# Kernel optimization log

Measured on AMD Instinct MI355X. Metric: run time of the kernel, lower is better.

## Reference

```python
import jax, jax.numpy as jnp
import numpy as np

N = 512      # state dim n
K = 8        # num_regimes
H = 256      # hidden dim for g0/g1/gate MLPs
B = 8192     # batch
INIT_SCALE = 0.1


def _mlp(x, w1, b1, w2, b2, w3, b3):
    # 2 hidden SiLU layers + linear head (matches ScalarMLP/GateNet with num_layers=2)
    h = jax.nn.silu(x @ w1 + b1)
    h = jax.nn.silu(h @ w2 + b2)
    return h @ w3 + b3


def setup_inputs() -> dict:
    key = jax.random.key(0)
    ks = jax.random.split(key, 12)

    def lin(k, fi, fo):
        kw, kb = jax.random.split(k)
        s = 1.0 / np.sqrt(fi)  # torch nn.Linear default init range
        w = jax.random.uniform(kw, (fi, fo), minval=-s, maxval=s, dtype=jnp.float32)
        b = jax.random.uniform(kb, (fo,), minval=-s, maxval=s, dtype=jnp.float32)
        return w, b

    g0_w1, g0_b1 = lin(ks[0], N, H)
    g0_w2, g0_b2 = lin(ks[1], H, H)
    g0_w3, g0_b3 = lin(ks[2], H, 1)
    g1_w1, g1_b1 = lin(ks[3], N, H)
    g1_w2, g1_b2 = lin(ks[4], H, H)
    g1_w3, g1_b3 = lin(ks[5], H, 1)
    gt_w1, gt_b1 = lin(ks[6], N, H)
    gt_w2, gt_b2 = lin(ks[7], H, H)
    gt_w3, gt_b3 = lin(ks[8], H, K)
    W = jax.random.uniform(ks[9], (K, N, N), minval=-INIT_SCALE, maxval=INIT_SCALE, dtype=jnp.float32)
    z = jax.random.normal(ks[10], (B, 2 * N), dtype=jnp.float32)
    return dict(z=z,
                g0_w1=g0_w1, g0_b1=g0_b1, g0_w2=g0_w2, g0_b2=g0_b2, g0_w3=g0_w3, g0_b3=g0_b3,
                g1_w1=g1_w1, g1_b1=g1_b1, g1_w2=g1_w2, g1_b2=g1_b2, g1_w3=g1_w3, g1_b3=g1_b3,
                gt_w1=gt_w1, gt_b1=gt_b1, gt_w2=gt_w2, gt_b2=gt_b2, gt_w3=gt_w3, gt_b3=gt_b3,
                W=W)


def reference(z,
              g0_w1, g0_b1, g0_w2, g0_b2, g0_w3, g0_b3,
              g1_w1, g1_b1, g1_w2, g1_b2, g1_w3, g1_b3,
              gt_w1, gt_b1, gt_w2, gt_b2, gt_w3, gt_b3,
              W):
    n = W.shape[-1]
    x0, x1 = z[:, :n], z[:, n:]

    def U(x0_, x1_):
        e0 = jnp.sum(_mlp(x0_, g0_w1, g0_b1, g0_w2, g0_b2, g0_w3, g0_b3))  # scalar
        e1 = jnp.sum(_mlp(x1_, g1_w1, g1_b1, g1_w2, g1_b2, g1_w3, g1_b3))
        alpha = jax.nn.softmax(_mlp(x0_, gt_w1, gt_b1, gt_w2, gt_b2, gt_w3, gt_b3), axis=-1)  # [B,K]
        # per-sample per-regime bilinear x1^T W_k x0 -> avoids materializing [B,n,n] W_eff
        q = jnp.einsum('bi,kij,bj->bk', x1_, W, x0_)
        return e0 + e1 + jnp.sum(alpha * q)

    grad_x0, grad_x1 = jax.grad(U, argnums=(0, 1))(x0, x1)
    return jnp.concatenate([-grad_x0, -grad_x1], axis=-1)  # [B, 2n]
```

## Files before the change

kernel.cpp:

```cpp
#include <hip/hip_runtime.h>
#include <cstdint>
#include <cstddef>

constexpr int BTOT = 8192, N = 512, H = 256, K = 8;

typedef __attribute__((ext_vector_type(8))) short short8v;
typedef __attribute__((ext_vector_type(4))) float f32x4;

__device__ __forceinline__ float bf2f(unsigned short u) {
    return __uint_as_float(((uint32_t)u) << 16);
}
__device__ __forceinline__ unsigned short f2bf(float f) {
    uint32_t u = __float_as_uint(f);
    uint32_t r = (u + 0x7FFFu + ((u >> 16) & 1u)) >> 16;
    return (unsigned short)r;
}

typedef __attribute__((address_space(3))) unsigned int lds_uint;
typedef __attribute__((address_space(1))) const unsigned int glob_uint;
__device__ __forceinline__ void async16(const unsigned short* g, unsigned short* l) {
    __builtin_amdgcn_global_load_lds((glob_uint*)g, (lds_uint*)l, 16, 0, 0);
}

struct GArg {
    const unsigned short* A;
    const unsigned short* Bt;
    const float* bias;
    const float* w3v;
    const unsigned short* dmul;
    unsigned short* ob;
    unsigned short* ob2;
    float* of;
    float* qout;
    const unsigned short* xq;
    int lda, ldbt, Ka, lddm, ldob, ldof;
};

enum { EPI_BF = 0, EPI_FWD = 1, EPI_BWD2 = 2, EPI_NEG = 3, EPI_NEGW = 4 };

template<int EPI>
__global__ __launch_bounds__(256) void gemm_g(GArg ga0, GArg ga1, GArg ga2)
{
    const int z = blockIdx.z;
    const GArg g = (z == 0) ? ga0 : (z == 1) ? ga1 : ga2;

    __shared__ __attribute__((aligned(16))) unsigned short As[3 * 128 * 32];
    __shared__ __attribute__((aligned(16))) unsigned short Bs[3 * 128 * 32];
    const int tid = threadIdx.x;
    const int lane = tid & 63, wave = tid >> 6;
    const int m0 = blockIdx.y * 128, n0 = blockIdx.x * 128;
    const int wr = (wave >> 1) * 64, wc = (wave & 1) * 64;
    const int rr = lane & 15;
    const int kb = ((lane >> 4) ^ (lane & 3)) << 3;

    const int r0 = tid >> 2;
    const int ko0 = (((tid & 3) ^ (r0 & 3)) << 3);
    const unsigned short* gA0 = g.A + (size_t)(m0 + r0) * g.lda + ko0;
    const unsigned short* gA1 = g.A + (size_t)(m0 + r0 + 64) * g.lda + ko0;
    const unsigned short* gB0 = g.Bt + (size_t)(n0 + r0) * g.ldbt + ko0;
    const unsigned short* gB1 = g.Bt + (size_t)(n0 + r0 + 64) * g.ldbt + ko0;

    auto stage = [&](int t, int buf) {
        const int k0 = t << 5;
        async16(gA0 + k0, As + buf * 4096 + tid * 8);
        async16(gA1 + k0, As + buf * 4096 + (tid + 256) * 8);
        async16(gB0 + k0, Bs + buf * 4096 + tid * 8);
        async16(gB1 + k0, Bs + buf * 4096 + (tid + 256) * 8);
    };

    f32x4 acc[4][4];
    #pragma unroll
    for (int i = 0; i < 4; ++i)
        #pragma unroll
        for (int j = 0; j < 4; ++j) acc[i][j] = (f32x4){0.f, 0.f, 0.f, 0.f};

    const int nt = g.Ka >> 5;

    stage(0, 0);
    if (nt > 1) stage(1, 1);

    int buf = 0;
    for (int t = 0; t < nt; ++t) {
        if (t + 1 < nt) { asm volatile("s_waitcnt vmcnt(4)" ::: "memory"); }
        else            { asm volatile("s_waitcnt vmcnt(0)" ::: "memory"); }
        __builtin_amdgcn_s_barrier();
        if (t + 2 < nt) {
            int b2 = buf + 2; if (b2 >= 3) b2 -= 3;
            stage(t + 2, b2);
        }
        short8v af[4], bfr[4];
        #pragma unroll
        for (int i = 0; i < 4; ++i)
            af[i] = *(const short8v*)(As + buf * 4096 + (wr + i * 16 + rr) * 32 + kb);
        #pragma unroll
        for (int j = 0; j < 4; ++j)
            bfr[j] = *(const short8v*)(Bs + buf * 4096 + (wc + j * 16 + rr) * 32 + kb);
        #pragma unroll
        for (int i = 0; i < 4; ++i)
            #pragma unroll
            for (int j = 0; j < 4; ++j)
                acc[i][j] = __builtin_amdgcn_mfma_f32_16x16x32_bf16(af[i], bfr[j], acc[i][j], 0, 0, 0);
        if (++buf == 3) buf = 0;
    }

    const int orow = (lane >> 4) * 4;
    #pragma unroll
    for (int i = 0; i < 4; ++i) {
        #pragma unroll
        for (int e = 0; e < 4; ++e) {
            const int row = m0 + wr + i * 16 + orow + e;
            #pragma unroll
            for (int j = 0; j < 4; ++j) {
                const int col = n0 + wc + rr + j * 16;
                float v = acc[i][j][e];
                if constexpr (EPI == EPI_BF) {
                    g.ob[(size_t)row * g.ldob + col] = f2bf(v);
                } else if constexpr (EPI == EPI_FWD) {
                    float p = v + g.bias[col];
                    float s = 1.f / (1.f + expf(-p));
                    if (g.ob) g.ob[(size_t)row * g.ldob + col] = f2bf(p * s);
                    float ds = s * (1.f + p * (1.f - s));
                    if (g.w3v) ds *= g.w3v[col];
                    g.ob2[(size_t)row * g.ldob + col] = f2bf(ds);
                } else if constexpr (EPI == EPI_BWD2) {
                    float t = v * bf2f(g.dmul[(size_t)row * g.lddm + col]);
                    g.ob[(size_t)row * g.ldob + col] = f2bf(t);
                } else if constexpr (EPI == EPI_NEG) {
                    g.of[(size_t)row * g.ldof + col] -= v;
                } else {
                    g.of[(size_t)row * g.ldof + col] = -v;
                }
            }
        }
    }

    if constexpr (EPI == EPI_BF) {
        if (g.qout) {
            const int kq = n0 >> 9, i0 = n0 & 511;
            __syncthreads();
            #pragma unroll
            for (int it = 0; it < 8; ++it) {
                int ci = tid + it * 256;
                int rg = ci >> 4, co = (ci & 15) << 3;
                const unsigned short* src = g.xq + (size_t)(m0 + rg) * 1024 + i0 + co;
                unsigned short* dst = (it < 4 ? As : Bs) + (rg & 63) * 128 + co;
                async16(src, dst);
            }
            asm volatile("s_waitcnt vmcnt(0)" ::: "memory");
            __builtin_amdgcn_s_barrier();
            const unsigned short* half = (wr == 0) ? As : Bs;
            #pragma unroll
            for (int i = 0; i < 4; ++i) {
                #pragma unroll
                for (int e = 0; e < 4; ++e) {
                    const int rl = i * 16 + orow + e;
                    float sq = 0.f;
                    #pragma unroll
                    for (int j = 0; j < 4; ++j)
                        sq += acc[i][j][e] * bf2f(half[rl * 128 + wc + rr + j * 16]);
                    sq += __shfl_xor(sq, 1, 64);
                    sq += __shfl_xor(sq, 2, 64);
                    sq += __shfl_xor(sq, 4, 64);
                    sq += __shfl_xor(sq, 8, 64);
                    if (rr == 0)
                        atomicAdd(g.qout + (size_t)(m0 + wr + rl) * K + kq, sq);
                }
            }
        }
    }
}

__global__ __launch_bounds__(256) void k_cvt_z(const float* __restrict__ z,
                                               unsigned short* __restrict__ o) {
    int g = (blockIdx.x * 256 + threadIdx.x) * 4;
    float4 v = *(const float4*)(z + g);
    ushort4 u;
    u.x = f2bf(v.x); u.y = f2bf(v.y); u.z = f2bf(v.z); u.w = f2bf(v.w);
    *(ushort4*)(o + g) = u;
}

__global__ __launch_bounds__(256) void k_transpose_w(const float* __restrict__ W,
    unsigned short* __restrict__ Wbf, unsigned short* __restrict__ WTbf)
{
    __shared__ float t[32][33];
    int k = blockIdx.z;
    int i0 = blockIdx.y * 32, j0 = blockIdx.x * 32;
    int tj = threadIdx.x & 31, ti = threadIdx.x >> 5;
    const float* Wk = W + (size_t)k * N * N;
    #pragma unroll
    for (int r = 0; r < 32; r += 8) {
        float v = Wk[(size_t)(i0 + ti + r) * N + j0 + tj];
        t[ti + r][tj] = v;
        Wbf[(size_t)k * N * N + (size_t)(i0 + ti + r) * N + j0 + tj] = f2bf(v);
    }
    __syncthreads();
    #pragma unroll
    for (int r = 0; r < 32; r += 8)
        WTbf[(size_t)k * N * N + (size_t)(j0 + ti + r) * N + i0 + tj] = f2bf(t[tj][ti + r]);
}

struct CvtJob { const float* src; unsigned short* dst; int ls, ld, cols32, tiles, trans; };
struct CvtTable { CvtJob j[12]; };

__global__ __launch_bounds__(256) void k_cvt_w(CvtTable T)
{
    int t = blockIdx.x;
    int ji = 0;
    while (t >= T.j[ji].tiles) { t -= T.j[ji].tiles; ++ji; }
    CvtJob jb = T.j[ji];
    int i0 = (t / jb.cols32) * 32, c0 = (t % jb.cols32) * 32;
    int tc = threadIdx.x & 31, tr = threadIdx.x >> 5;
    if (!jb.trans) {
        #pragma unroll
        for (int r = 0; r < 32; r += 8)
            jb.dst[(size_t)(i0 + tr + r) * jb.ld + c0 + tc] =
                f2bf(jb.src[(size_t)(i0 + tr + r) * jb.ls + c0 + tc]);
    } else {
        __shared__ float tt[32][33];
        #pragma unroll
        for (int r = 0; r < 32; r += 8)
            tt[tr + r][tc] = jb.src[(size_t)(i0 + tr + r) * jb.ls + c0 + tc];
        __syncthreads();
        #pragma unroll
        for (int r = 0; r < 32; r += 8)
            jb.dst[(size_t)(c0 + tr + r) * jb.ld + i0 + tc] = f2bf(tt[tc][tr + r]);
    }
}

__global__ __launch_bounds__(256) void k_head_s(const unsigned short* __restrict__ h2t,
    const float* __restrict__ w3t, const float* __restrict__ b3t,
    float* __restrict__ s)
{
    int t = threadIdx.x;
    int bl = t >> 3, k = t & 7;
    int b = blockIdx.x * 32 + bl;
    const unsigned short* ar = h2t + (size_t)b * H;
    float acc = b3t[k];
    for (int h0 = 0; h0 < H; h0 += 8) {
        short8v hv = *(const short8v*)(ar + h0);
        #pragma unroll
        for (int u = 0; u < 8; ++u)
            acc += bf2f((unsigned short)hv[u]) * w3t[(h0 + u) * K + k];
    }
    s[b * K + k] = acc;
}

__global__ __launch_bounds__(256) void k_q(const unsigned short* __restrict__ v0,
    const unsigned short* __restrict__ zb, float* __restrict__ q)
{
    int w = threadIdx.x >> 6, lane = threadIdx.x & 63;
    int idx = blockIdx.x * 4 + w;
    int b = idx >> 3, k = idx & 7;
    const unsigned short* vr = v0 + ((size_t)b * K + k) * N;
    const unsigned short* xr = zb + (size_t)b * 1024 + 512;
    short8v vv = *(const short8v*)(vr + lane * 8);
    short8v xv = *(const short8v*)(xr + lane * 8);
    float s = 0.f;
    #pragma unroll
    for (int t = 0; t < 8; ++t)
        s += bf2f((unsigned short)vv[t]) * bf2f((unsigned short)xv[t]);
    for (int off = 32; off; off >>= 1) s += __shfl_down(s, off, 64);
    if (lane == 0) q[idx] = s;
}

__global__ __launch_bounds__(256) void k_d(const float* __restrict__ s,
    const float* __restrict__ q, float* __restrict__ alpha,
    float* __restrict__ dd, int Bc)
{
    int b = blockIdx.x * 256 + threadIdx.x;
    if (b >= Bc) return;
    float sv[K], qv[K];
    float m = -1e30f;
    #pragma unroll
    for (int k = 0; k < K; ++k) { sv[k] = s[b * K + k]; m = fmaxf(m, sv[k]); }
    float sum = 0.f;
    #pragma unroll
    for (int k = 0; k < K; ++k) { sv[k] = expf(sv[k] - m); sum += sv[k]; }
    float inv = 1.f / sum, qbar = 0.f;
    #pragma unroll
    for (int k = 0; k < K; ++k) { sv[k] *= inv; qv[k] = q[b * K + k]; qbar += sv[k] * qv[k]; }
    #pragma unroll
    for (int k = 0; k < K; ++k) {
        alpha[b * K + k] = sv[k];
        dd[b * K + k] = sv[k] * (qv[k] - qbar);
    }
}

__global__ __launch_bounds__(256) void k_u2t(
    const unsigned short* __restrict__ d2_t,
    const float* __restrict__ w3t, const float* __restrict__ dd,
    unsigned short* __restrict__ u2_t)
{
    int g = blockIdx.x * 256 + threadIdx.x;
    int h = g & (H - 1), b = g >> 8;
    float s = 0.f;
    #pragma unroll
    for (int k = 0; k < K; ++k) s += w3t[h * K + k] * dd[b * K + k];
    u2_t[g] = f2bf(s * bf2f(d2_t[g]));
}

__global__ __launch_bounds__(256) void k_gxq2(const unsigned short* __restrict__ v0,
    const unsigned short* __restrict__ v1, const float* __restrict__ alpha,
    float* __restrict__ out)
{
    int g = blockIdx.x * 256 + threadIdx.x;
    int b = g >> 6, jb = (g & 63) << 3;
    float al[K];
    #pragma unroll
    for (int k = 0; k < K; ++k) al[k] = alpha[b * K + k];
    const unsigned short* pv0 = v0 + (size_t)b * K * N + jb;
    const unsigned short* pv1 = v1 + (size_t)b * K * N + jb;
    float s0[8] = {}, s1[8] = {};
    #pragma unroll
    for (int k = 0; k < K; ++k) {
        short8v w1 = *(const short8v*)(pv1 + (size_t)k * N);
        short8v w0 = *(const short8v*)(pv0 + (size_t)k * N);
        #pragma unroll
        for (int t = 0; t < 8; ++t) {
            s0[t] += al[k] * bf2f((unsigned short)w1[t]);
            s1[t] += al[k] * bf2f((unsigned short)w0[t]);
        }
    }
    float* o0 = out + (size_t)b * 1024 + jb;
    float* o1 = o0 + 512;
    float4 x0 = *(float4*)o0, x1 = *(float4*)(o0 + 4);
    x0.x -= s0[0]; x0.y -= s0[1]; x0.z -= s0[2]; x0.w -= s0[3];
    x1.x -= s0[4]; x1.y -= s0[5]; x1.z -= s0[6]; x1.w -= s0[7];
    *(float4*)o0 = x0; *(float4*)(o0 + 4) = x1;
    float4 y0 = *(float4*)o1, y1 = *(float4*)(o1 + 4);
    y0.x -= s1[0]; y0.y -= s1[1]; y0.z -= s1[2]; y0.w -= s1[3];
    y1.x -= s1[4]; y1.y -= s1[5]; y1.z -= s1[6]; y1.w -= s1[7];
    *(float4*)o1 = y0; *(float4*)(o1 + 4) = y1;
}

extern "C" void kernel_launch(void* const* d_in, const int* in_sizes, int n_in,
                              void* d_out, int out_size, void* d_ws, size_t ws_size,
                              hipStream_t stream) {
    const float* z     = (const float*)d_in[0];
    const float* g0_w1 = (const float*)d_in[1];  const float* g0_b1 = (const float*)d_in[2];
    const float* g0_w2 = (const float*)d_in[3];  const float* g0_b2 = (const float*)d_in[4];
    const float* g0_w3 = (const float*)d_in[5];
    const float* g1_w1 = (const float*)d_in[7];  const float* g1_b1 = (const float*)d_in[8];
    const float* g1_w2 = (const float*)d_in[9];  const float* g1_b2 = (const float*)d_in[10];
    const float* g1_w3 = (const float*)d_in[11];
    const float* gt_w1 = (const float*)d_in[13]; const float* gt_b1 = (const float*)d_in[14];
    const float* gt_w2 = (const float*)d_in[15]; const float* gt_b2 = (const float*)d_in[16];
    const float* gt_w3 = (const float*)d_in[17]; const float* gt_b3 = (const float*)d_in[18];
    const float* W     = (const float*)d_in[19];
    float* out = (float*)d_out;

    char* wsb = (char*)d_ws;
    size_t off = 0;
    auto aus = [&](size_t n) -> unsigned short* {
        unsigned short* r = (unsigned short*)(wsb + off);
        off += ((n * 2 + 255) & ~(size_t)255);
        return r;
    };
    auto af4 = [&](size_t n) -> float* {
        float* r = (float*)(wsb + off);
        off += ((n * 4 + 255) & ~(size_t)255);
        return r;
    };

    unsigned short* Zbf  = aus((size_t)BTOT * 1024);
    unsigned short* Wbf  = aus((size_t)K * N * N);
    unsigned short* WTbf = aus((size_t)K * N * N);
    unsigned short* w1T[3], *w2T[3], *w2N[3];
    for (int i = 0; i < 3; ++i) w1T[i] = aus((size_t)H * N);
    for (int i = 0; i < 3; ++i) w2T[i] = aus((size_t)H * H);
    for (int i = 0; i < 3; ++i) w2N[i] = aus((size_t)H * H);
    unsigned short* w1N1  = aus((size_t)N * H);
    unsigned short* w1cat = aus((size_t)N * 2 * H);
    unsigned short* h1[3], *d1b[3], *u2[3];
    for (int i = 0; i < 3; ++i) h1[i]  = aus((size_t)BTOT * H);
    for (int i = 0; i < 3; ++i) d1b[i] = aus((size_t)BTOT * H);
    for (int i = 0; i < 3; ++i) u2[i]  = aus((size_t)BTOT * H);
    unsigned short* d2t   = aus((size_t)BTOT * H);
    unsigned short* h2t   = aus((size_t)BTOT * H);
    unsigned short* t2cat = aus((size_t)BTOT * 512);
    unsigned short* t21   = aus((size_t)BTOT * H);
    float* sbuf = af4((size_t)BTOT * K);
    float* qbuf = af4((size_t)BTOT * K);
    float* abuf = af4((size_t)BTOT * K);
    float* dbuf = af4((size_t)BTOT * K);

    int Bcv = BTOT;
    while (off + 2 * (((size_t)Bcv * K * N * 2 + 255) & ~(size_t)255) > ws_size && Bcv > 128)
        Bcv >>= 1;
    unsigned short* v0 = aus((size_t)Bcv * K * N);
    unsigned short* v1 = aus((size_t)Bcv * K * N);
    const bool full = (Bcv == BTOT);

    const dim3 blk(256);

    if (!full)
        hipMemsetAsync(d_out, 0, (size_t)out_size * sizeof(float), stream);
    if (full)
        hipMemsetAsync(qbuf, 0, (size_t)BTOT * K * sizeof(float), stream);

    k_cvt_z<<<BTOT * 1024 / (256 * 4), blk, 0, stream>>>(z, Zbf);
    k_transpose_w<<<dim3(N / 32, N / 32, K), blk, 0, stream>>>(W, Wbf, WTbf);

    CvtTable T;
    int nj = 0, tot = 0;
    auto addjob = [&](const float* src, int ls, unsigned short* dst, int ld,
                      int rows, int cols, int trans) {
        CvtJob jb; jb.src = src; jb.dst = dst; jb.ls = ls; jb.ld = ld;
        jb.cols32 = cols / 32; jb.tiles = (rows / 32) * (cols / 32); jb.trans = trans;
        T.j[nj++] = jb; tot += jb.tiles;
    };
    addjob(g0_w1, H, w1T[0], N, N, H, 1);
    addjob(g1_w1, H, w1T[1], N, N, H, 1);
    addjob(gt_w1, H, w1T[2], N, N, H, 1);
    addjob(g0_w2, H, w2T[0], H, H, H, 1);
    addjob(g1_w2, H, w2T[1], H, H, H, 1);
    addjob(gt_w2, H, w2T[2], H, H, H, 1);
    addjob(g0_w2, H, w2N[0], H, H, H, 0);
    addjob(g1_w2, H, w2N[1], H, H, H, 0);
    addjob(gt_w2, H, w2N[2], H, H, H, 0);
    addjob(g1_w1, H, w1N1, H, N, H, 0);
    addjob(g0_w1, H, w1cat, 2 * H, N, H, 0);
    addjob(gt_w1, H, w1cat + H, 2 * H, N, H, 0);
    k_cvt_w<<<tot, blk, 0, stream>>>(T);

    auto mk = [](const unsigned short* A, int lda, const unsigned short* Bt, int ldbt, int Ka) {
        GArg g; g.A = A; g.Bt = Bt; g.bias = nullptr; g.w3v = nullptr; g.dmul = nullptr;
        g.ob = nullptr; g.ob2 = nullptr; g.of = nullptr;
        g.qout = nullptr; g.xq = nullptr;
        g.lda = lda; g.ldbt = ldbt; g.Ka = Ka; g.lddm = 0; g.ldob = 0; g.ldof = 0;
        return g;
    };

    {
        const float* bs[3] = {g0_b1, g1_b1, gt_b1};
        GArg a[3];
        for (int i = 0; i < 3; ++i) {
            a[i] = mk(Zbf + (i == 1 ? 512 : 0), 1024, w1T[i], N, N);
            a[i].bias = bs[i]; a[i].ob = h1[i]; a[i].ob2 = d1b[i]; a[i].ldob = H;
        }
        gemm_g<EPI_FWD><<<dim3(H / 128, BTOT / 128, 3), blk, 0, stream>>>(a[0], a[1], a[2]);
    }
    {
        const float* bs[3] = {g0_b2, g1_b2, gt_b2};
        const float* w3[3] = {g0_w3, g1_w3, nullptr};
        GArg a[3];
        for (int i = 0; i < 3; ++i) {
            a[i] = mk(h1[i], H, w2T[i], H, H);
            a[i].bias = bs[i];
            a[i].w3v = w3[i];
            a[i].ob  = (i == 2) ? h2t : nullptr;
            a[i].ob2 = (i == 2) ? d2t : u2[i];
            a[i].ldob = H;
        }
        gemm_g<EPI_FWD><<<dim3(H / 128, BTOT / 128, 3), blk, 0, stream>>>(a[0], a[1], a[2]);
    }
    k_head_s<<<BTOT / 32, blk, 0, stream>>>(h2t, gt_w3, gt_b3, sbuf);

    for (int cb = 0; cb < BTOT; cb += Bcv) {
        GArg a[2];
        a[0] = mk(Zbf + (size_t)cb * 1024, 1024, Wbf, N, N);
        a[0].ob = v0; a[0].ldob = K * N;
        if (full) {
            a[0].qout = qbuf;
            a[0].xq = Zbf + 512;
        }
        a[1] = mk(Zbf + (size_t)cb * 1024 + 512, 1024, WTbf, N, N);
        a[1].ob = v1; a[1].ldob = K * N;
        gemm_g<EPI_BF><<<dim3(K * N / 128, Bcv / 128, 2), blk, 0, stream>>>(a[0], a[1], a[1]);

        if (!full)
            k_q<<<Bcv * K / 4, blk, 0, stream>>>(v0, Zbf + (size_t)cb * 1024, qbuf + (size_t)cb * K);
        k_d<<<(Bcv + 255) / 256, blk, 0, stream>>>(sbuf + (size_t)cb * K, qbuf + (size_t)cb * K,
                                                   abuf + (size_t)cb * K, dbuf + (size_t)cb * K, Bcv);
        if (!full)
            k_gxq2<<<Bcv * 64 / 256, blk, 0, stream>>>(v0, v1, abuf + (size_t)cb * K,
                                                       out + (size_t)cb * 1024);
    }

    k_u2t<<<BTOT * H / 256, blk, 0, stream>>>(d2t, gt_w3, dbuf, u2[2]);

    {
        GArg a[3];
        a[0] = mk(u2[0], H, w2N[0], H, H);
        a[0].dmul = d1b[0]; a[0].lddm = H; a[0].ob = t2cat;     a[0].ldob = 512;
        a[1] = mk(u2[1], H, w2N[1], H, H);
        a[1].dmul = d1b[1]; a[1].lddm = H; a[1].ob = t21;       a[1].ldob = H;
        a[2] = mk(u2[2], H, w2N[2], H, H);
        a[2].dmul = d1b[2]; a[2].lddm = H; a[2].ob = t2cat + H; a[2].ldob = 512;
        gemm_g<EPI_BWD2><<<dim3(H / 128, BTOT / 128, 3), blk, 0, stream>>>(a[0], a[1], a[2]);
    }
    {
        GArg a[2];
        a[0] = mk(t2cat, 512, w1cat, 2 * H, 512);
        a[0].of = out;       a[0].ldof = 1024;
        a[1] = mk(t21, H, w1N1, H, H);
        a[1].of = out + 512; a[1].ldof = 1024;
        if (full) {
            gemm_g<EPI_NEGW><<<dim3(N / 128, BTOT / 128, 2), blk, 0, stream>>>(a[0], a[1], a[1]);
            k_gxq2<<<BTOT * 64 / 256, blk, 0, stream>>>(v0, v1, abuf, out);
        } else {
            gemm_g<EPI_NEG><<<dim3(N / 128, BTOT / 128, 2), blk, 0, stream>>>(a[0], a[1], a[1]);
        }
    }
}
```

Baseline: 276.4 us.

## Merge prep kernels into one launch and compute q with separate kernel

Merges the z conversion, W transpose and weight conversion kernels into a single k_prep launch, removing two launches. It also drops the fused q-reduction epilogue (LDS reload plus atomics) from the bilinear GEMM and the qbuf memset, and always computes q with the standalone k_q kernel. This shortens the GEMM tail and removes atomics, at the cost of k_q re-reading v0 from memory.

```diff
diff --git a/kernel.cpp b/kernel.cpp
--- a/kernel.cpp
+++ b/kernel.cpp
@@ -31,8 +31,6 @@
     unsigned short* ob;
     unsigned short* ob2;
     float* of;
-    float* qout;
-    const unsigned short* xq;
     int lda, ldbt, Ka, lddm, ldob, ldof;
 };
 
@@ -133,97 +131,65 @@
             }
         }
     }
-
-    if constexpr (EPI == EPI_BF) {
-        if (g.qout) {
-            const int kq = n0 >> 9, i0 = n0 & 511;
-            __syncthreads();
-            #pragma unroll
-            for (int it = 0; it < 8; ++it) {
-                int ci = tid + it * 256;
-                int rg = ci >> 4, co = (ci & 15) << 3;
-                const unsigned short* src = g.xq + (size_t)(m0 + rg) * 1024 + i0 + co;
-                unsigned short* dst = (it < 4 ? As : Bs) + (rg & 63) * 128 + co;
-                async16(src, dst);
-            }
-            asm volatile("s_waitcnt vmcnt(0)" ::: "memory");
-            __builtin_amdgcn_s_barrier();
-            const unsigned short* half = (wr == 0) ? As : Bs;
-            #pragma unroll
-            for (int i = 0; i < 4; ++i) {
-                #pragma unroll
-                for (int e = 0; e < 4; ++e) {
-                    const int rl = i * 16 + orow + e;
-                    float sq = 0.f;
-                    #pragma unroll
-                    for (int j = 0; j < 4; ++j)
-                        sq += acc[i][j][e] * bf2f(half[rl * 128 + wc + rr + j * 16]);
-                    sq += __shfl_xor(sq, 1, 64);
-                    sq += __shfl_xor(sq, 2, 64);
-                    sq += __shfl_xor(sq, 4, 64);
-                    sq += __shfl_xor(sq, 8, 64);
-                    if (rr == 0)
-                        atomicAdd(g.qout + (size_t)(m0 + wr + rl) * K + kq, sq);
-                }
-            }
-        }
-    }
-}
-
-__global__ __launch_bounds__(256) void k_cvt_z(const float* __restrict__ z,
-                                               unsigned short* __restrict__ o) {
-    int g = (blockIdx.x * 256 + threadIdx.x) * 4;
-    float4 v = *(const float4*)(z + g);
-    ushort4 u;
-    u.x = f2bf(v.x); u.y = f2bf(v.y); u.z = f2bf(v.z); u.w = f2bf(v.w);
-    *(ushort4*)(o + g) = u;
-}
-
-__global__ __launch_bounds__(256) void k_transpose_w(const float* __restrict__ W,
-    unsigned short* __restrict__ Wbf, unsigned short* __restrict__ WTbf)
-{
-    __shared__ float t[32][33];
-    int k = blockIdx.z;
-    int i0 = blockIdx.y * 32, j0 = blockIdx.x * 32;
-    int tj = threadIdx.x & 31, ti = threadIdx.x >> 5;
-    const float* Wk = W + (size_t)k * N * N;
-    #pragma unroll
-    for (int r = 0; r < 32; r += 8) {
-        float v = Wk[(size_t)(i0 + ti + r) * N + j0 + tj];
-        t[ti + r][tj] = v;
-        Wbf[(size_t)k * N * N + (size_t)(i0 + ti + r) * N + j0 + tj] = f2bf(v);
-    }
-    __syncthreads();
-    #pragma unroll
-    for (int r = 0; r < 32; r += 8)
-        WTbf[(size_t)k * N * N + (size_t)(j0 + ti + r) * N + i0 + tj] = f2bf(t[tj][ti + r]);
 }
 
 struct CvtJob { const float* src; unsigned short* dst; int ls, ld, cols32, tiles, trans; };
 struct CvtTable { CvtJob j[12]; };
 
-__global__ __launch_bounds__(256) void k_cvt_w(CvtTable T)
-{
-    int t = blockIdx.x;
+constexpr int PREP_ZB = BTOT * 1024 / (256 * 4);
+constexpr int PREP_TW = (N / 32) * (N / 32) * K;
+
+__global__ __launch_bounds__(256) void k_prep(const float* __restrict__ z,
+    unsigned short* __restrict__ Zbf, const float* __restrict__ W,
+    unsigned short* __restrict__ Wbf, unsigned short* __restrict__ WTbf,
+    CvtTable T)
+{
+    __shared__ float t[32][33];
+    int bid = blockIdx.x;
+    if (bid < PREP_ZB) {
+        int g = (bid * 256 + threadIdx.x) * 4;
+        float4 v = *(const float4*)(z + g);
+        ushort4 u;
+        u.x = f2bf(v.x); u.y = f2bf(v.y); u.z = f2bf(v.z); u.w = f2bf(v.w);
+        *(ushort4*)(Zbf + g) = u;
+        return;
+    }
+    bid -= PREP_ZB;
+    int tc = threadIdx.x & 31, tr = threadIdx.x >> 5;
+    if (bid < PREP_TW) {
+        int k = bid >> 8, rem = bid & 255;
+        int i0 = (rem >> 4) * 32, j0 = (rem & 15) * 32;
+        const float* Wk = W + (size_t)k * N * N;
+        #pragma unroll
+        for (int r = 0; r < 32; r += 8) {
+            float v = Wk[(size_t)(i0 + tr + r) * N + j0 + tc];
+            t[tr + r][tc] = v;
+            Wbf[(size_t)k * N * N + (size_t)(i0 + tr + r) * N + j0 + tc] = f2bf(v);
+        }
+        __syncthreads();
+        #pragma unroll
+        for (int r = 0; r < 32; r += 8)
+            WTbf[(size_t)k * N * N + (size_t)(j0 + tr + r) * N + i0 + tc] = f2bf(t[tc][tr + r]);
+        return;
+    }
+    bid -= PREP_TW;
     int ji = 0;
-    while (t >= T.j[ji].tiles) { t -= T.j[ji].tiles; ++ji; }
+    while (bid >= T.j[ji].tiles) { bid -= T.j[ji].tiles; ++ji; }
     CvtJob jb = T.j[ji];
-    int i0 = (t / jb.cols32) * 32, c0 = (t % jb.cols32) * 32;
-    int tc = threadIdx.x & 31, tr = threadIdx.x >> 5;
+    int i0 = (bid / jb.cols32) * 32, c0 = (bid % jb.cols32) * 32;
     if (!jb.trans) {
         #pragma unroll
         for (int r = 0; r < 32; r += 8)
             jb.dst[(size_t)(i0 + tr + r) * jb.ld + c0 + tc] =
                 f2bf(jb.src[(size_t)(i0 + tr + r) * jb.ls + c0 + tc]);
     } else {
-        __shared__ float tt[32][33];
         #pragma unroll
         for (int r = 0; r < 32; r += 8)
-            tt[tr + r][tc] = jb.src[(size_t)(i0 + tr + r) * jb.ls + c0 + tc];
+            t[tr + r][tc] = jb.src[(size_t)(i0 + tr + r) * jb.ls + c0 + tc];
         __syncthreads();
         #pragma unroll
         for (int r = 0; r < 32; r += 8)
-            jb.dst[(size_t)(c0 + tr + r) * jb.ld + i0 + tc] = f2bf(tt[tc][tr + r]);
+            jb.dst[(size_t)(c0 + tr + r) * jb.ld + i0 + tc] = f2bf(t[tc][tr + r]);
     }
 }
 
@@ -395,11 +361,6 @@
 
     if (!full)
         hipMemsetAsync(d_out, 0, (size_t)out_size * sizeof(float), stream);
-    if (full)
-        hipMemsetAsync(qbuf, 0, (size_t)BTOT * K * sizeof(float), stream);
-
-    k_cvt_z<<<BTOT * 1024 / (256 * 4), blk, 0, stream>>>(z, Zbf);
-    k_transpose_w<<<dim3(N / 32, N / 32, K), blk, 0, stream>>>(W, Wbf, WTbf);
 
     CvtTable T;
     int nj = 0, tot = 0;
@@ -421,12 +382,11 @@
     addjob(g1_w1, H, w1N1, H, N, H, 0);
     addjob(g0_w1, H, w1cat, 2 * H, N, H, 0);
     addjob(gt_w1, H, w1cat + H, 2 * H, N, H, 0);
-    k_cvt_w<<<tot, blk, 0, stream>>>(T);
+    k_prep<<<PREP_ZB + PREP_TW + tot, blk, 0, stream>>>(z, Zbf, W, Wbf, WTbf, T);
 
     auto mk = [](const unsigned short* A, int lda, const unsigned short* Bt, int ldbt, int Ka) {
         GArg g; g.A = A; g.Bt = Bt; g.bias = nullptr; g.w3v = nullptr; g.dmul = nullptr;
         g.ob = nullptr; g.ob2 = nullptr; g.of = nullptr;
-        g.qout = nullptr; g.xq = nullptr;
         g.lda = lda; g.ldbt = ldbt; g.Ka = Ka; g.lddm = 0; g.ldob = 0; g.ldof = 0;
         return g;
     };
@@ -460,16 +420,11 @@
         GArg a[2];
         a[0] = mk(Zbf + (size_t)cb * 1024, 1024, Wbf, N, N);
         a[0].ob = v0; a[0].ldob = K * N;
-        if (full) {
-            a[0].qout = qbuf;
-            a[0].xq = Zbf + 512;
-        }
         a[1] = mk(Zbf + (size_t)cb * 1024 + 512, 1024, WTbf, N, N);
         a[1].ob = v1; a[1].ldob = K * N;
         gemm_g<EPI_BF><<<dim3(K * N / 128, Bcv / 128, 2), blk, 0, stream>>>(a[0], a[1], a[1]);
 
-        if (!full)
-            k_q<<<Bcv * K / 4, blk, 0, stream>>>(v0, Zbf + (size_t)cb * 1024, qbuf + (size_t)cb * K);
+        k_q<<<Bcv * K / 4, blk, 0, stream>>>(v0, Zbf + (size_t)cb * 1024, qbuf + (size_t)cb * K);
         k_d<<<(Bcv + 255) / 256, blk, 0, stream>>>(sbuf + (size_t)cb * K, qbuf + (size_t)cb * K,
                                                    abuf + (size_t)cb * K, dbuf + (size_t)cb * K, Bcv);
         if (!full)
```

Measured after the change: 259.5 us. 1.07x faster.
